# Performance work log

Hardware: AMD Instinct MI355X
Metric: run time of the kernel (lower is better)

## Reference

```python
import jax, jax.numpy as jnp
import numpy as np

N_NODES = 20000
N_EDGES = 320000
D_IN = 128
D_HID = 128
D_OUT = 128
HEADS = 4
NEG_SLOPE = 0.2
BN_EPS = 1e-5


def _gat_conv(x, src, dst, W, a_src, a_dst, b):
    """PyG GATConv with concat=False (mean over heads). Self-loops already in src/dst."""
    N = x.shape[0]
    H, C = a_src.shape
    h = (x @ W).reshape(N, H, C)                     # [N,H,C] per-head projections
    alpha_s = jnp.sum(h * a_src, axis=-1)            # [N,H]
    alpha_d = jnp.sum(h * a_dst, axis=-1)            # [N,H]
    logits = jax.nn.leaky_relu(alpha_s[src] + alpha_d[dst], NEG_SLOPE)  # [E,H]
    # segment softmax over incoming edges of each destination node
    m = jax.ops.segment_max(logits, dst, num_segments=N)               # [N,H]
    e = jnp.exp(logits - m[dst])
    z = jax.ops.segment_sum(e, dst, num_segments=N)                     # [N,H]
    alpha = e / (z[dst] + 1e-16)                                        # [E,H]
    msg = h[src] * alpha[:, :, None]                                    # [E,H,C]
    out = jax.ops.segment_sum(msg, dst, num_segments=N)                 # [N,H,C]
    return jnp.mean(out, axis=1) + b                                    # [N,C]


def _bn(x, gamma, beta):
    mu = jnp.mean(x, axis=0)
    var = jnp.var(x, axis=0)
    return (x - mu) * jax.lax.rsqrt(var + BN_EPS) * gamma + beta


def setup_inputs() -> dict:
    key = jax.random.key(0)
    ks = jax.random.split(key, 24)
    inp = {
        'x': jax.random.normal(ks[0], (N_NODES, D_IN), jnp.float32),
        'edge_index': jax.random.randint(ks[1], (2, N_EDGES), 0, N_NODES, jnp.int64),
        'edge_attr': jax.random.normal(ks[2], (N_EDGES, 16), jnp.float32),
    }
    def glorot(k, shape):
        fan = sum(shape) if len(shape) > 1 else shape[0]
        return jax.random.normal(k, shape, jnp.float32) * np.float32(np.sqrt(2.0 / fan))
    dims = [(D_IN, D_HID), (D_HID, D_HID), (D_HID, D_OUT)]
    for i, (din, dout) in enumerate(dims):
        inp[f'W{i}'] = glorot(ks[3 + 4 * i], (din, HEADS * dout))
        inp[f'asrc{i}'] = glorot(ks[4 + 4 * i], (HEADS, dout))
        inp[f'adst{i}'] = glorot(ks[5 + 4 * i], (HEADS, dout))
        inp[f'b{i}'] = jnp.zeros((dout,), jnp.float32)
    for i in range(2):
        inp[f'gamma{i}'] = jnp.ones((D_HID,), jnp.float32)
        inp[f'beta{i}'] = jnp.zeros((D_HID,), jnp.float32)
    return inp


def reference(x, edge_index, edge_attr, W0, asrc0, adst0, b0, gamma0, beta0,
              W1, asrc1, adst1, b1, gamma1, beta1, W2, asrc2, adst2, b2):
    N = x.shape[0]
    ar = jnp.arange(N, dtype=edge_index.dtype)
    src = jnp.concatenate([edge_index[0], ar])  # add self-loops (PyG default)
    dst = jnp.concatenate([edge_index[1], ar])
    h = _gat_conv(x, src, dst, W0, asrc0, adst0, b0)
    h = jax.nn.relu(_bn(h, gamma0, beta0))
    h = _gat_conv(h, src, dst, W1, asrc1, adst1, b1)
    h = jax.nn.relu(_bn(h, gamma1, beta1))
    out = _gat_conv(h, src, dst, W2, asrc2, adst2, b2)
    return (out, edge_attr)
```

## Files before the change

kernel.cpp:

```cpp
#include <hip/hip_runtime.h>
#include <hip/hip_fp16.h>
#include <math.h>

#define N_NODES 20000
#define N_EDGES 320000
#define EN (N_EDGES + N_NODES)
#define DIM 128
#define HEADS 4
#define DH (HEADS * DIM)
#define NEG_SLOPE 0.2f
#define BN_EPS 1e-5f

typedef _Float16 h4 __attribute__((ext_vector_type(4)));
typedef _Float16 h8 __attribute__((ext_vector_type(8)));
typedef float f4 __attribute__((ext_vector_type(4)));

__device__ __forceinline__ float lrelu(float x) { return x > 0.f ? x : NEG_SLOPE * x; }


__global__ __launch_bounds__(256) void build_edges_kernel(
    const void* __restrict__ ei_raw, int* __restrict__ src32,
    int* __restrict__ dst32, int* __restrict__ deg) {
  int e = blockIdx.x * 256 + threadIdx.x;
  if (e >= EN) return;
  const long long* ei64 = (const long long*)ei_raw;
  const int* ei32 = (const int*)ei_raw;
  bool is64 = true;
#pragma unroll
  for (int k = 0; k < 4; ++k) {
    long long v = ei64[k];
    if (v < 0 || v >= N_NODES) is64 = false;
  }
  int s, d;
  if (e < N_EDGES) {
    if (is64) { s = (int)ei64[e]; d = (int)ei64[N_EDGES + e]; }
    else      { s = ei32[e];      d = ei32[N_EDGES + e]; }
  } else {
    s = d = e - N_EDGES;
  }
  src32[e] = s;
  dst32[e] = d;
  atomicAdd(&deg[d], 1);
}

__global__ __launch_bounds__(1024) void scan_kernel(
    const int* __restrict__ deg, int* __restrict__ off) {
  __shared__ int sums[1024];
  const int tid = threadIdx.x;
  const int chunk = (N_NODES + 1023) / 1024;
  int start = tid * chunk;
  int end = start + chunk; if (end > N_NODES) end = N_NODES;
  int s = 0;
  for (int i = start; i < end && i < N_NODES; ++i) s += deg[i];
  sums[tid] = s;
  __syncthreads();
  for (int st = 1; st < 1024; st <<= 1) {
    int t = (tid >= st) ? sums[tid - st] : 0;
    __syncthreads();
    sums[tid] += t;
    __syncthreads();
  }
  int run = sums[tid] - s;
  for (int i = start; i < end && i < N_NODES; ++i) { off[i] = run; run += deg[i]; }
  if (tid == 1023) off[N_NODES] = sums[1023];
}

__global__ __launch_bounds__(256) void scatter_kernel(
    const int* __restrict__ src32, const int* __restrict__ dst32,
    const int* __restrict__ off, int* __restrict__ cursor,
    int* __restrict__ csrc) {
  int e = blockIdx.x * 256 + threadIdx.x;
  if (e >= EN) return;
  int d = dst32[e];
  int pos = atomicAdd(&cursor[d], 1);
  csrc[off[d] + pos] = src32[e];
}


__global__ __launch_bounds__(128) void wtrans_kernel(
    const float* __restrict__ W0, const float* __restrict__ W1,
    const float* __restrict__ W2, __half* __restrict__ T0,
    __half* __restrict__ T1, __half* __restrict__ T2) {
  int n = blockIdx.x;
  int k = threadIdx.x;
  const float* W = (blockIdx.y == 0) ? W0 : (blockIdx.y == 1) ? W1 : W2;
  __half* T = (blockIdx.y == 0) ? T0 : (blockIdx.y == 1) ? T1 : T2;
  T[(size_t)n * 128 + k] = __float2half(W[(size_t)k * 512 + n]);
}


__global__ __launch_bounds__(128) void bn_coef_kernel(
    const float* __restrict__ stats, const float* __restrict__ gamma,
    const float* __restrict__ beta, float* __restrict__ coef) {
  int c = threadIdx.x;
  const float invN = 1.f / (float)N_NODES;
  float mean = stats[c] * invN;
  float var = stats[DIM + c] * invN - mean * mean;
  float scale = gamma[c] * rsqrtf(var + BN_EPS);
  coef[c] = scale;
  coef[DIM + c] = beta[c] - mean * scale;
}


#define SWZ(r, byte_in_row) (((r) * 256 + (byte_in_row)) ^ (((r) & 7) << 4))

__global__ __launch_bounds__(256) void gemm_fused_kernel(
    const float* __restrict__ A, const __half* __restrict__ Wt,
    const float* __restrict__ coef, int apply_bn,
    const float* __restrict__ a_src, const float* __restrict__ a_dst,
    ushort* __restrict__ H16, float* __restrict__ as_,
    float* __restrict__ ad_, int M) {
  __shared__ __align__(16) char Xt[64 * 256];
  __shared__ __align__(16) char Wl[64 * 256];
  __shared__ float red_as[4][4][2][16];
  __shared__ float red_ad[4][4][2][16];
  int tid = threadIdx.x;
  int brow = blockIdx.x * 64;
  int half_id = blockIdx.y;
  const float4* coef4 = (const float4*)coef;
#pragma unroll
  for (int it = 0; it < 8; ++it) {
    int idx = it * 256 + tid;
    int r = idx >> 5, c4 = idx & 31;
    int row = brow + r;
    float4 v = make_float4(0.f, 0.f, 0.f, 0.f);
    if (row < M) {
      v = *(const float4*)&A[(size_t)row * 128 + c4 * 4];
      if (apply_bn) {
        float4 sc = coef4[c4], sh = coef4[32 + c4];
        v.x = fmaxf(v.x * sc.x + sh.x, 0.f);
        v.y = fmaxf(v.y * sc.y + sh.y, 0.f);
        v.z = fmaxf(v.z * sc.z + sh.z, 0.f);
        v.w = fmaxf(v.w * sc.w + sh.w, 0.f);
      }
    }
    h4 hv;
    hv[0] = (_Float16)v.x; hv[1] = (_Float16)v.y;
    hv[2] = (_Float16)v.z; hv[3] = (_Float16)v.w;
    *(h4*)(Xt + SWZ(r, c4 * 8)) = hv;
  }
  int wave = tid >> 6, lane = tid & 63;
  int lrow = lane & 15, kgrp = lane >> 4;
  float asum[4][2] = {}, adsum[4][2] = {};
  for (int nc = 0; nc < 4; ++nc) {
    int chunk = half_id * 4 + nc;
    int hh = nc >> 1;
    __syncthreads();
#pragma unroll
    for (int it = 0; it < 4; ++it) {
      int idx = it * 256 + tid;
      int r = idx >> 4, c4 = idx & 15;
      uint4 v = *(const uint4*)&Wt[(size_t)(chunk * 64 + r) * 128 + c4 * 8];
      *(uint4*)(Wl + SWZ(r, c4 * 16)) = v;
    }
    __syncthreads();
    f4 acc[4] = {};
#pragma unroll
    for (int ks = 0; ks < 4; ++ks) {
      int kb = ks * 64 + kgrp * 16;
      h8 af = *(h8*)(Wl + SWZ(wave * 16 + lrow, kb));
#pragma unroll
      for (int mt = 0; mt < 4; ++mt) {
        h8 bf = *(h8*)(Xt + SWZ(mt * 16 + lrow, kb));
        acc[mt] = __builtin_amdgcn_mfma_f32_16x16x32_f16(af, bf, acc[mt], 0, 0, 0);
      }
    }
    int n_base = chunk * 64 + wave * 16 + kgrp * 4;
    float4 as4 = *(const float4*)&a_src[n_base];
    float4 ad4 = *(const float4*)&a_dst[n_base];
#pragma unroll
    for (int mt = 0; mt < 4; ++mt) {
      int m = brow + mt * 16 + lrow;
      if (m < M) {
        h4 hv;
#pragma unroll
        for (int i = 0; i < 4; ++i) hv[i] = (_Float16)acc[mt][i];
        *(h4*)&H16[(size_t)m * DH + n_base] = hv;
      }
      asum[mt][hh] += acc[mt][0] * as4.x + acc[mt][1] * as4.y +
                      acc[mt][2] * as4.z + acc[mt][3] * as4.w;
      adsum[mt][hh] += acc[mt][0] * ad4.x + acc[mt][1] * ad4.y +
                       acc[mt][2] * ad4.z + acc[mt][3] * ad4.w;
    }
  }
#pragma unroll
  for (int mt = 0; mt < 4; ++mt)
#pragma unroll
    for (int hh = 0; hh < 2; ++hh) {
      asum[mt][hh] += __shfl_xor(asum[mt][hh], 16);
      asum[mt][hh] += __shfl_xor(asum[mt][hh], 32);
      adsum[mt][hh] += __shfl_xor(adsum[mt][hh], 16);
      adsum[mt][hh] += __shfl_xor(adsum[mt][hh], 32);
    }
  __syncthreads();
  if (lane < 16) {
#pragma unroll
    for (int mt = 0; mt < 4; ++mt)
#pragma unroll
      for (int hh = 0; hh < 2; ++hh) {
        red_as[wave][mt][hh][lrow] = asum[mt][hh];
        red_ad[wave][mt][hh][lrow] = adsum[mt][hh];
      }
  }
  __syncthreads();
  if (tid < 128) {
    int mt = tid >> 5, hh = (tid >> 4) & 1, lr = tid & 15;
    float s = red_as[0][mt][hh][lr] + red_as[1][mt][hh][lr] +
              red_as[2][mt][hh][lr] + red_as[3][mt][hh][lr];
    float d = red_ad[0][mt][hh][lr] + red_ad[1][mt][hh][lr] +
              red_ad[2][mt][hh][lr] + red_ad[3][mt][hh][lr];
    int m = brow + mt * 16 + lr;
    if (m < M) {
      int head = half_id * 2 + hh;
      as_[m * 4 + head] = s;
      ad_[m * 4 + head] = d;
    }
  }
}


__global__ __launch_bounds__(256) void smagg_kernel(
    const ushort* __restrict__ H16, const float* __restrict__ as_,
    const float* __restrict__ ad_, const int* __restrict__ off,
    const int* __restrict__ csrc, const float* __restrict__ bias,
    float* __restrict__ out, float* __restrict__ galpha) {
  __shared__ float alds[4][64 * 4];
  int tid = threadIdx.x;
  int slot = tid >> 6;
  int n = blockIdx.x * 4 + slot;
  int lane = tid & 63;
  int e0 = off[n], e1 = off[n + 1];
  int deg = e1 - e0;
  bool fast = (deg <= 64);
  float4 ad = *(const float4*)&ad_[n * 4];
  if (fast) {
    bool valid = lane < deg;
    float l0 = -1e30f, l1 = -1e30f, l2 = -1e30f, l3 = -1e30f;
    if (valid) {
      int s = csrc[e0 + lane];
      float4 av = *(const float4*)&as_[s * 4];
      l0 = lrelu(av.x + ad.x); l1 = lrelu(av.y + ad.y);
      l2 = lrelu(av.z + ad.z); l3 = lrelu(av.w + ad.w);
    }
    float m0 = l0, m1 = l1, m2 = l2, m3 = l3;
#pragma unroll
    for (int o = 32; o > 0; o >>= 1) {
      m0 = fmaxf(m0, __shfl_xor(m0, o)); m1 = fmaxf(m1, __shfl_xor(m1, o));
      m2 = fmaxf(m2, __shfl_xor(m2, o)); m3 = fmaxf(m3, __shfl_xor(m3, o));
    }
    float p0 = valid ? expf(l0 - m0) : 0.f;
    float p1 = valid ? expf(l1 - m1) : 0.f;
    float p2 = valid ? expf(l2 - m2) : 0.f;
    float p3 = valid ? expf(l3 - m3) : 0.f;
    float z0 = p0, z1 = p1, z2 = p2, z3 = p3;
#pragma unroll
    for (int o = 32; o > 0; o >>= 1) {
      z0 += __shfl_xor(z0, o); z1 += __shfl_xor(z1, o);
      z2 += __shfl_xor(z2, o); z3 += __shfl_xor(z3, o);
    }
    if (valid) {
      float4 r = make_float4(p0 / (z0 + 1e-16f), p1 / (z1 + 1e-16f),
                             p2 / (z2 + 1e-16f), p3 / (z3 + 1e-16f));
      *(float4*)&alds[slot][lane * 4] = r;
    }
  } else {
    float m0 = -1e30f, m1 = -1e30f, m2 = -1e30f, m3 = -1e30f;
    for (int i = e0 + lane; i < e1; i += 64) {
      int s = csrc[i];
      float4 av = *(const float4*)&as_[s * 4];
      float l0 = lrelu(av.x + ad.x), l1 = lrelu(av.y + ad.y);
      float l2 = lrelu(av.z + ad.z), l3 = lrelu(av.w + ad.w);
      ((float4*)galpha)[i] = make_float4(l0, l1, l2, l3);
      m0 = fmaxf(m0, l0); m1 = fmaxf(m1, l1);
      m2 = fmaxf(m2, l2); m3 = fmaxf(m3, l3);
    }
#pragma unroll
    for (int o = 32; o > 0; o >>= 1) {
      m0 = fmaxf(m0, __shfl_xor(m0, o)); m1 = fmaxf(m1, __shfl_xor(m1, o));
      m2 = fmaxf(m2, __shfl_xor(m2, o)); m3 = fmaxf(m3, __shfl_xor(m3, o));
    }
    float z0 = 0.f, z1 = 0.f, z2 = 0.f, z3 = 0.f;
    for (int i = e0 + lane; i < e1; i += 64) {
      float4 l = ((const float4*)galpha)[i];
      float p0 = expf(l.x - m0), p1 = expf(l.y - m1);
      float p2 = expf(l.z - m2), p3 = expf(l.w - m3);
      ((float4*)galpha)[i] = make_float4(p0, p1, p2, p3);
      z0 += p0; z1 += p1; z2 += p2; z3 += p3;
    }
#pragma unroll
    for (int o = 32; o > 0; o >>= 1) {
      z0 += __shfl_xor(z0, o); z1 += __shfl_xor(z1, o);
      z2 += __shfl_xor(z2, o); z3 += __shfl_xor(z3, o);
    }
    float r0 = 1.f / (z0 + 1e-16f), r1 = 1.f / (z1 + 1e-16f);
    float r2 = 1.f / (z2 + 1e-16f), r3 = 1.f / (z3 + 1e-16f);
    for (int i = e0 + lane; i < e1; i += 64) {
      float4 p = ((const float4*)galpha)[i];
      ((float4*)galpha)[i] = make_float4(p.x * r0, p.y * r1, p.z * r2, p.w * r3);
    }
  }
  const uint4* Hp = (const uint4*)H16;
  const float* af = &alds[slot][0];
  int head = lane >> 4;
  float acc[8] = {};
#define AGG_BODY(ii)                                                       \
  {                                                                        \
    int s = csrc[ii];                                                      \
    float w = fast ? af[((ii) - e0) * 4 + head]                            \
                   : galpha[(size_t)(ii) * 4 + head];                      \
    uint4 hv = Hp[(size_t)s * 64 + lane];                                  \
    float2 f0 = __half22float2(*(__half2*)&hv.x);                          \
    float2 f1 = __half22float2(*(__half2*)&hv.y);                          \
    float2 f2 = __half22float2(*(__half2*)&hv.z);                          \
    float2 f3 = __half22float2(*(__half2*)&hv.w);                          \
    acc[0] += w * f0.x; acc[1] += w * f0.y;                                \
    acc[2] += w * f1.x; acc[3] += w * f1.y;                                \
    acc[4] += w * f2.x; acc[5] += w * f2.y;                                \
    acc[6] += w * f3.x; acc[7] += w * f3.y;                                \
  }
  int i = e0;
  for (; i + 7 < e1; i += 8) {
    AGG_BODY(i)     AGG_BODY(i + 1) AGG_BODY(i + 2) AGG_BODY(i + 3)
    AGG_BODY(i + 4) AGG_BODY(i + 5) AGG_BODY(i + 6) AGG_BODY(i + 7)
  }
  for (; i < e1; ++i) AGG_BODY(i)
#undef AGG_BODY
#pragma unroll
  for (int j = 0; j < 8; ++j) {
    acc[j] += __shfl_xor(acc[j], 16);
    acc[j] += __shfl_xor(acc[j], 32);
  }
  if (lane < 16) {
    int c0 = lane * 8;
    float4 b0 = *(const float4*)&bias[c0];
    float4 b1 = *(const float4*)&bias[c0 + 4];
    float4 r0 = make_float4(0.25f * acc[0] + b0.x, 0.25f * acc[1] + b0.y,
                            0.25f * acc[2] + b0.z, 0.25f * acc[3] + b0.w);
    float4 r1 = make_float4(0.25f * acc[4] + b1.x, 0.25f * acc[5] + b1.y,
                            0.25f * acc[6] + b1.z, 0.25f * acc[7] + b1.w);
    *(float4*)&out[(size_t)n * DIM + c0] = r0;
    *(float4*)&out[(size_t)n * DIM + c0 + 4] = r1;
  }
}


__global__ __launch_bounds__(256) void bn_stats_kernel(
    const float* __restrict__ X, float* __restrict__ stats) {
  int c = threadIdx.x & 127;
  int hlf = threadIdx.x >> 7;
  float s = 0.f, s2 = 0.f;
  for (int r = blockIdx.x * 2 + hlf; r < N_NODES; r += gridDim.x * 2) {
    float v = X[(size_t)r * DIM + c];
    s += v;
    s2 += v * v;
  }
  atomicAdd(&stats[c], s);
  atomicAdd(&stats[DIM + c], s2);
}


extern "C" void kernel_launch(void* const* d_in, const int* in_sizes, int n_in,
                              void* d_out, int out_size, void* d_ws, size_t ws_size,
                              hipStream_t stream) {
  (void)in_sizes; (void)n_in; (void)out_size; (void)ws_size;
  const float* x = (const float*)d_in[0];
  const void* ei = d_in[1];
  const float* eattr = (const float*)d_in[2];
  const float* W[3]    = {(const float*)d_in[3],  (const float*)d_in[7],  (const float*)d_in[11]};
  const float* asrc[3] = {(const float*)d_in[4],  (const float*)d_in[8],  (const float*)d_in[12]};
  const float* adst[3] = {(const float*)d_in[5],  (const float*)d_in[9],  (const float*)d_in[13]};
  const float* bias[3] = {(const float*)d_in[6],  (const float*)d_in[10], (const float*)d_in[14]};
  const float* gamma[2] = {(const float*)d_in[15], (const float*)d_in[17]};
  const float* beta[2]  = {(const float*)d_in[16], (const float*)d_in[18]};

  char* ws = (char*)d_ws;
  size_t o = 0;
  auto alloc = [&](size_t bytes) -> void* {
    void* p = ws + o;
    o += (bytes + 255) & ~(size_t)255;
    return p;
  };
  int* deg      = (int*)alloc(N_NODES * 4);
  int* cursor   = (int*)alloc(N_NODES * 4);
  float* stats0 = (float*)alloc(2 * DIM * 4);
  float* stats1 = (float*)alloc(2 * DIM * 4);
  size_t zero_bytes = o;
  int* off    = (int*)alloc((N_NODES + 1) * 4);
  int* src32  = (int*)alloc((size_t)EN * 4);
  int* dst32  = (int*)alloc((size_t)EN * 4);
  int* csrc   = (int*)alloc((size_t)EN * 4);
  float* galpha = (float*)alloc((size_t)EN * 4 * 4);
  ushort* H16  = (ushort*)alloc((size_t)N_NODES * DH * 2);
  float* Ob    = (float*)alloc((size_t)N_NODES * DIM * 4);
  float* as_   = (float*)alloc((size_t)N_NODES * 4 * 4);
  float* ad_   = (float*)alloc((size_t)N_NODES * 4 * 4);
  float* coef0 = (float*)alloc(2 * DIM * 4);
  float* coef1 = (float*)alloc(2 * DIM * 4);
  __half* Wt[3];
  for (int L = 0; L < 3; ++L) Wt[L] = (__half*)alloc((size_t)DH * 128 * 2);

  hipMemsetAsync(d_ws, 0, zero_bytes, stream);

  build_edges_kernel<<<(EN + 255) / 256, 256, 0, stream>>>(ei, src32, dst32, deg);
  scan_kernel<<<1, 1024, 0, stream>>>(deg, off);
  scatter_kernel<<<(EN + 255) / 256, 256, 0, stream>>>(src32, dst32, off, cursor, csrc);
  wtrans_kernel<<<dim3(DH, 3), 128, 0, stream>>>(W[0], W[1], W[2], Wt[0], Wt[1], Wt[2]);

  const float* in_ptr = x;
  const float* coefs[3] = {coef0, coef0, coef1};
  for (int L = 0; L < 3; ++L) {
    gemm_fused_kernel<<<dim3((N_NODES + 63) / 64, 2), 256, 0, stream>>>(
        in_ptr, Wt[L], coefs[L], (L > 0) ? 1 : 0, asrc[L], adst[L],
        H16, as_, ad_, N_NODES);
    float* outp = (L == 2) ? (float*)d_out : Ob;
    smagg_kernel<<<N_NODES / 4, 256, 0, stream>>>(H16, as_, ad_, off, csrc,
                                                  bias[L], outp, galpha);
    if (L < 2) {
      float* st = (L == 0) ? stats0 : stats1;
      float* cf = (L == 0) ? coef0 : coef1;
      bn_stats_kernel<<<256, 256, 0, stream>>>(Ob, st);
      bn_coef_kernel<<<1, 128, 0, stream>>>(st, gamma[L], beta[L], cf);
      in_ptr = Ob;
    }
  }

  hipMemcpyAsync((float*)d_out + (size_t)N_NODES * DIM, eattr,
                 (size_t)N_EDGES * 16 * 4, hipMemcpyDeviceToDevice, stream);
}
```

Measured before the change: 444.6 us.

## Double-buffer GEMM weight tiles over all heads and split aggregation across two waves

The fused GEMM kernel now handles all eight 64-column weight chunks in one block instead of splitting heads over two blocks. It stages each next weight chunk in registers and double-buffers it in LDS, which removes the duplicate X staging and overlaps weight loads with MFMA work. The aggregation kernel uses two waves per node, each handling alternate edges, and combines their partial sums through LDS. This raises memory-level parallelism for the gather but adds block barriers and halves the GEMM grid, which may reduce occupancy.

Result: slower. 526.2 us (+18.4%).

```diff
diff --git a/kernel.cpp b/kernel.cpp
--- a/kernel.cpp
+++ b/kernel.cpp
@@ -111,12 +111,11 @@
     ushort* __restrict__ H16, float* __restrict__ as_,
     float* __restrict__ ad_, int M) {
   __shared__ __align__(16) char Xt[64 * 256];
-  __shared__ __align__(16) char Wl[64 * 256];
-  __shared__ float red_as[4][4][2][16];
-  __shared__ float red_ad[4][4][2][16];
+  __shared__ __align__(16) char Wl[2][64 * 256];
+  __shared__ float red_as[4][4][4][16];
+  __shared__ float red_ad[4][4][4][16];
   int tid = threadIdx.x;
   int brow = blockIdx.x * 64;
-  int half_id = blockIdx.y;
   const float4* coef4 = (const float4*)coef;
 #pragma unroll
   for (int it = 0; it < 8; ++it) {
@@ -140,32 +139,37 @@
     *(h4*)(Xt + SWZ(r, c4 * 8)) = hv;
   }
   int wave = tid >> 6, lane = tid & 63;
+  int wr = tid >> 4, wc4 = tid & 15;
   int lrow = lane & 15, kgrp = lane >> 4;
-  float asum[4][2] = {}, adsum[4][2] = {};
-  for (int nc = 0; nc < 4; ++nc) {
-    int chunk = half_id * 4 + nc;
+  float asum[4][4] = {}, adsum[4][4] = {};
+  uint4 wreg[4];
+#pragma unroll
+  for (int it = 0; it < 4; ++it)
+    wreg[it] = *(const uint4*)&Wt[(size_t)(it * 16 + wr) * 128 + wc4 * 8];
+  for (int nc = 0; nc < 8; ++nc) {
+    char* buf = Wl[nc & 1];
     int hh = nc >> 1;
+#pragma unroll
+    for (int it = 0; it < 4; ++it)
+      *(uint4*)(buf + SWZ(it * 16 + wr, wc4 * 16)) = wreg[it];
     __syncthreads();
-#pragma unroll
-    for (int it = 0; it < 4; ++it) {
-      int idx = it * 256 + tid;
-      int r = idx >> 4, c4 = idx & 15;
-      uint4 v = *(const uint4*)&Wt[(size_t)(chunk * 64 + r) * 128 + c4 * 8];
-      *(uint4*)(Wl + SWZ(r, c4 * 16)) = v;
-    }
-    __syncthreads();
+    if (nc < 7) {
+#pragma unroll
+      for (int it = 0; it < 4; ++it)
+        wreg[it] = *(const uint4*)&Wt[(size_t)((nc + 1) * 64 + it * 16 + wr) * 128 + wc4 * 8];
+    }
     f4 acc[4] = {};
 #pragma unroll
     for (int ks = 0; ks < 4; ++ks) {
       int kb = ks * 64 + kgrp * 16;
-      h8 af = *(h8*)(Wl + SWZ(wave * 16 + lrow, kb));
+      h8 af = *(h8*)(buf + SWZ(wave * 16 + lrow, kb));
 #pragma unroll
       for (int mt = 0; mt < 4; ++mt) {
         h8 bf = *(h8*)(Xt + SWZ(mt * 16 + lrow, kb));
         acc[mt] = __builtin_amdgcn_mfma_f32_16x16x32_f16(af, bf, acc[mt], 0, 0, 0);
       }
     }
-    int n_base = chunk * 64 + wave * 16 + kgrp * 4;
+    int n_base = nc * 64 + wave * 16 + kgrp * 4;
     float4 as4 = *(const float4*)&a_src[n_base];
     float4 ad4 = *(const float4*)&a_dst[n_base];
 #pragma unroll
@@ -182,123 +186,128 @@
       adsum[mt][hh] += acc[mt][0] * ad4.x + acc[mt][1] * ad4.y +
                        acc[mt][2] * ad4.z + acc[mt][3] * ad4.w;
     }
+    __syncthreads();
   }
 #pragma unroll
   for (int mt = 0; mt < 4; ++mt)
 #pragma unroll
-    for (int hh = 0; hh < 2; ++hh) {
+    for (int hh = 0; hh < 4; ++hh) {
       asum[mt][hh] += __shfl_xor(asum[mt][hh], 16);
       asum[mt][hh] += __shfl_xor(asum[mt][hh], 32);
       adsum[mt][hh] += __shfl_xor(adsum[mt][hh], 16);
       adsum[mt][hh] += __shfl_xor(adsum[mt][hh], 32);
     }
-  __syncthreads();
   if (lane < 16) {
 #pragma unroll
     for (int mt = 0; mt < 4; ++mt)
 #pragma unroll
-      for (int hh = 0; hh < 2; ++hh) {
+      for (int hh = 0; hh < 4; ++hh) {
         red_as[wave][mt][hh][lrow] = asum[mt][hh];
         red_ad[wave][mt][hh][lrow] = adsum[mt][hh];
       }
   }
   __syncthreads();
-  if (tid < 128) {
-    int mt = tid >> 5, hh = (tid >> 4) & 1, lr = tid & 15;
+  {
+    int mt = tid >> 6, hh = (tid >> 4) & 3, lr = tid & 15;
     float s = red_as[0][mt][hh][lr] + red_as[1][mt][hh][lr] +
               red_as[2][mt][hh][lr] + red_as[3][mt][hh][lr];
     float d = red_ad[0][mt][hh][lr] + red_ad[1][mt][hh][lr] +
               red_ad[2][mt][hh][lr] + red_ad[3][mt][hh][lr];
     int m = brow + mt * 16 + lr;
     if (m < M) {
-      int head = half_id * 2 + hh;
-      as_[m * 4 + head] = s;
-      ad_[m * 4 + head] = d;
-    }
-  }
-}
-
-
-__global__ __launch_bounds__(256) void smagg_kernel(
+      as_[m * 4 + hh] = s;
+      ad_[m * 4 + hh] = d;
+    }
+  }
+}
+
+
+__global__ __launch_bounds__(512) void smagg_kernel(
     const ushort* __restrict__ H16, const float* __restrict__ as_,
     const float* __restrict__ ad_, const int* __restrict__ off,
     const int* __restrict__ csrc, const float* __restrict__ bias,
     float* __restrict__ out, float* __restrict__ galpha) {
   __shared__ float alds[4][64 * 4];
+  __shared__ float pred[4][128];
   int tid = threadIdx.x;
-  int slot = tid >> 6;
+  int wave = tid >> 6;
+  int slot = wave >> 1;
+  int sub = wave & 1;
   int n = blockIdx.x * 4 + slot;
   int lane = tid & 63;
   int e0 = off[n], e1 = off[n + 1];
   int deg = e1 - e0;
   bool fast = (deg <= 64);
-  float4 ad = *(const float4*)&ad_[n * 4];
-  if (fast) {
-    bool valid = lane < deg;
-    float l0 = -1e30f, l1 = -1e30f, l2 = -1e30f, l3 = -1e30f;
-    if (valid) {
-      int s = csrc[e0 + lane];
-      float4 av = *(const float4*)&as_[s * 4];
-      l0 = lrelu(av.x + ad.x); l1 = lrelu(av.y + ad.y);
-      l2 = lrelu(av.z + ad.z); l3 = lrelu(av.w + ad.w);
-    }
-    float m0 = l0, m1 = l1, m2 = l2, m3 = l3;
-#pragma unroll
-    for (int o = 32; o > 0; o >>= 1) {
-      m0 = fmaxf(m0, __shfl_xor(m0, o)); m1 = fmaxf(m1, __shfl_xor(m1, o));
-      m2 = fmaxf(m2, __shfl_xor(m2, o)); m3 = fmaxf(m3, __shfl_xor(m3, o));
-    }
-    float p0 = valid ? expf(l0 - m0) : 0.f;
-    float p1 = valid ? expf(l1 - m1) : 0.f;
-    float p2 = valid ? expf(l2 - m2) : 0.f;
-    float p3 = valid ? expf(l3 - m3) : 0.f;
-    float z0 = p0, z1 = p1, z2 = p2, z3 = p3;
-#pragma unroll
-    for (int o = 32; o > 0; o >>= 1) {
-      z0 += __shfl_xor(z0, o); z1 += __shfl_xor(z1, o);
-      z2 += __shfl_xor(z2, o); z3 += __shfl_xor(z3, o);
-    }
-    if (valid) {
-      float4 r = make_float4(p0 / (z0 + 1e-16f), p1 / (z1 + 1e-16f),
-                             p2 / (z2 + 1e-16f), p3 / (z3 + 1e-16f));
-      *(float4*)&alds[slot][lane * 4] = r;
-    }
-  } else {
-    float m0 = -1e30f, m1 = -1e30f, m2 = -1e30f, m3 = -1e30f;
-    for (int i = e0 + lane; i < e1; i += 64) {
-      int s = csrc[i];
-      float4 av = *(const float4*)&as_[s * 4];
-      float l0 = lrelu(av.x + ad.x), l1 = lrelu(av.y + ad.y);
-      float l2 = lrelu(av.z + ad.z), l3 = lrelu(av.w + ad.w);
-      ((float4*)galpha)[i] = make_float4(l0, l1, l2, l3);
-      m0 = fmaxf(m0, l0); m1 = fmaxf(m1, l1);
-      m2 = fmaxf(m2, l2); m3 = fmaxf(m3, l3);
-    }
-#pragma unroll
-    for (int o = 32; o > 0; o >>= 1) {
-      m0 = fmaxf(m0, __shfl_xor(m0, o)); m1 = fmaxf(m1, __shfl_xor(m1, o));
-      m2 = fmaxf(m2, __shfl_xor(m2, o)); m3 = fmaxf(m3, __shfl_xor(m3, o));
-    }
-    float z0 = 0.f, z1 = 0.f, z2 = 0.f, z3 = 0.f;
-    for (int i = e0 + lane; i < e1; i += 64) {
-      float4 l = ((const float4*)galpha)[i];
-      float p0 = expf(l.x - m0), p1 = expf(l.y - m1);
-      float p2 = expf(l.z - m2), p3 = expf(l.w - m3);
-      ((float4*)galpha)[i] = make_float4(p0, p1, p2, p3);
-      z0 += p0; z1 += p1; z2 += p2; z3 += p3;
-    }
-#pragma unroll
-    for (int o = 32; o > 0; o >>= 1) {
-      z0 += __shfl_xor(z0, o); z1 += __shfl_xor(z1, o);
-      z2 += __shfl_xor(z2, o); z3 += __shfl_xor(z3, o);
-    }
-    float r0 = 1.f / (z0 + 1e-16f), r1 = 1.f / (z1 + 1e-16f);
-    float r2 = 1.f / (z2 + 1e-16f), r3 = 1.f / (z3 + 1e-16f);
-    for (int i = e0 + lane; i < e1; i += 64) {
-      float4 p = ((const float4*)galpha)[i];
-      ((float4*)galpha)[i] = make_float4(p.x * r0, p.y * r1, p.z * r2, p.w * r3);
-    }
-  }
+  if (sub == 0) {
+    float4 ad = *(const float4*)&ad_[n * 4];
+    if (fast) {
+      bool valid = lane < deg;
+      float l0 = -1e30f, l1 = -1e30f, l2 = -1e30f, l3 = -1e30f;
+      if (valid) {
+        int s = csrc[e0 + lane];
+        float4 av = *(const float4*)&as_[s * 4];
+        l0 = lrelu(av.x + ad.x); l1 = lrelu(av.y + ad.y);
+        l2 = lrelu(av.z + ad.z); l3 = lrelu(av.w + ad.w);
+      }
+      float m0 = l0, m1 = l1, m2 = l2, m3 = l3;
+#pragma unroll
+      for (int o = 32; o > 0; o >>= 1) {
+        m0 = fmaxf(m0, __shfl_xor(m0, o)); m1 = fmaxf(m1, __shfl_xor(m1, o));
+        m2 = fmaxf(m2, __shfl_xor(m2, o)); m3 = fmaxf(m3, __shfl_xor(m3, o));
+      }
+      float p0 = valid ? expf(l0 - m0) : 0.f;
+      float p1 = valid ? expf(l1 - m1) : 0.f;
+      float p2 = valid ? expf(l2 - m2) : 0.f;
+      float p3 = valid ? expf(l3 - m3) : 0.f;
+      float z0 = p0, z1 = p1, z2 = p2, z3 = p3;
+#pragma unroll
+      for (int o = 32; o > 0; o >>= 1) {
+        z0 += __shfl_xor(z0, o); z1 += __shfl_xor(z1, o);
+        z2 += __shfl_xor(z2, o); z3 += __shfl_xor(z3, o);
+      }
+      if (valid) {
+        float4 r = make_float4(p0 / (z0 + 1e-16f), p1 / (z1 + 1e-16f),
+                               p2 / (z2 + 1e-16f), p3 / (z3 + 1e-16f));
+        *(float4*)&alds[slot][lane * 4] = r;
+      }
+    } else {
+      float m0 = -1e30f, m1 = -1e30f, m2 = -1e30f, m3 = -1e30f;
+      for (int i = e0 + lane; i < e1; i += 64) {
+        int s = csrc[i];
+        float4 av = *(const float4*)&as_[s * 4];
+        float l0 = lrelu(av.x + ad.x), l1 = lrelu(av.y + ad.y);
+        float l2 = lrelu(av.z + ad.z), l3 = lrelu(av.w + ad.w);
+        ((float4*)galpha)[i] = make_float4(l0, l1, l2, l3);
+        m0 = fmaxf(m0, l0); m1 = fmaxf(m1, l1);
+        m2 = fmaxf(m2, l2); m3 = fmaxf(m3, l3);
+      }
+#pragma unroll
+      for (int o = 32; o > 0; o >>= 1) {
+        m0 = fmaxf(m0, __shfl_xor(m0, o)); m1 = fmaxf(m1, __shfl_xor(m1, o));
+        m2 = fmaxf(m2, __shfl_xor(m2, o)); m3 = fmaxf(m3, __shfl_xor(m3, o));
+      }
+      float z0 = 0.f, z1 = 0.f, z2 = 0.f, z3 = 0.f;
+      for (int i = e0 + lane; i < e1; i += 64) {
+        float4 l = ((const float4*)galpha)[i];
+        float p0 = expf(l.x - m0), p1 = expf(l.y - m1);
+        float p2 = expf(l.z - m2), p3 = expf(l.w - m3);
+        ((float4*)galpha)[i] = make_float4(p0, p1, p2, p3);
+        z0 += p0; z1 += p1; z2 += p2; z3 += p3;
+      }
+#pragma unroll
+      for (int o = 32; o > 0; o >>= 1) {
+        z0 += __shfl_xor(z0, o); z1 += __shfl_xor(z1, o);
+        z2 += __shfl_xor(z2, o); z3 += __shfl_xor(z3, o);
+      }
+      float r0 = 1.f / (z0 + 1e-16f), r1 = 1.f / (z1 + 1e-16f);
+      float r2 = 1.f / (z2 + 1e-16f), r3 = 1.f / (z3 + 1e-16f);
+      for (int i = e0 + lane; i < e1; i += 64) {
+        float4 p = ((const float4*)galpha)[i];
+        ((float4*)galpha)[i] = make_float4(p.x * r0, p.y * r1, p.z * r2, p.w * r3);
+      }
+    }
+  }
+  __syncthreads();
   const uint4* Hp = (const uint4*)H16;
   const float* af = &alds[slot][0];
   int head = lane >> 4;
@@ -318,26 +327,35 @@
     acc[4] += w * f2.x; acc[5] += w * f2.y;                                \
     acc[6] += w * f3.x; acc[7] += w * f3.y;                                \
   }
-  int i = e0;
-  for (; i + 7 < e1; i += 8) {
-    AGG_BODY(i)     AGG_BODY(i + 1) AGG_BODY(i + 2) AGG_BODY(i + 3)
-    AGG_BODY(i + 4) AGG_BODY(i + 5) AGG_BODY(i + 6) AGG_BODY(i + 7)
-  }
-  for (; i < e1; ++i) AGG_BODY(i)
+  int i = e0 + sub;
+  for (; i + 6 < e1; i += 8) {
+    AGG_BODY(i) AGG_BODY(i + 2) AGG_BODY(i + 4) AGG_BODY(i + 6)
+  }
+  for (; i < e1; i += 2) AGG_BODY(i)
 #undef AGG_BODY
 #pragma unroll
   for (int j = 0; j < 8; ++j) {
     acc[j] += __shfl_xor(acc[j], 16);
     acc[j] += __shfl_xor(acc[j], 32);
   }
-  if (lane < 16) {
+  if (sub == 1 && lane < 16) {
+#pragma unroll
+    for (int j = 0; j < 8; ++j) pred[slot][lane * 8 + j] = acc[j];
+  }
+  __syncthreads();
+  if (sub == 0 && lane < 16) {
     int c0 = lane * 8;
     float4 b0 = *(const float4*)&bias[c0];
     float4 b1 = *(const float4*)&bias[c0 + 4];
-    float4 r0 = make_float4(0.25f * acc[0] + b0.x, 0.25f * acc[1] + b0.y,
-                            0.25f * acc[2] + b0.z, 0.25f * acc[3] + b0.w);
-    float4 r1 = make_float4(0.25f * acc[4] + b1.x, 0.25f * acc[5] + b1.y,
-                            0.25f * acc[6] + b1.z, 0.25f * acc[7] + b1.w);
+    const float* pr = &pred[slot][c0];
+    float4 r0 = make_float4(0.25f * (acc[0] + pr[0]) + b0.x,
+                            0.25f * (acc[1] + pr[1]) + b0.y,
+                            0.25f * (acc[2] + pr[2]) + b0.z,
+                            0.25f * (acc[3] + pr[3]) + b0.w);
+    float4 r1 = make_float4(0.25f * (acc[4] + pr[4]) + b1.x,
+                            0.25f * (acc[5] + pr[5]) + b1.y,
+                            0.25f * (acc[6] + pr[6]) + b1.z,
+                            0.25f * (acc[7] + pr[7]) + b1.w);
     *(float4*)&out[(size_t)n * DIM + c0] = r0;
     *(float4*)&out[(size_t)n * DIM + c0 + 4] = r1;
   }
@@ -409,11 +427,11 @@
   const float* in_ptr = x;
   const float* coefs[3] = {coef0, coef0, coef1};
   for (int L = 0; L < 3; ++L) {
-    gemm_fused_kernel<<<dim3((N_NODES + 63) / 64, 2), 256, 0, stream>>>(
+    gemm_fused_kernel<<<(N_NODES + 63) / 64, 256, 0, stream>>>(
         in_ptr, Wt[L], coefs[L], (L > 0) ? 1 : 0, asrc[L], adst[L],
         H16, as_, ad_, N_NODES);
     float* outp = (L == 2) ? (float*)d_out : Ob;
-    smagg_kernel<<<N_NODES / 4, 256, 0, stream>>>(H16, as_, ad_, off, csrc,
+    smagg_kernel<<<N_NODES / 4, 512, 0, stream>>>(H16, as_, ad_, off, csrc,
                                                   bias[L], outp, galpha);
     if (L < 2) {
       float* st = (L == 0) ? stats0 : stats1;
```

## Pre-convert GEMM input to fp16 and load tiles via direct global-to-LDS loads

Applied to the files above, without the earlier changes.

Adds a separate kernel that applies the BN+ReLU and converts each layer's input to fp16 once, instead of doing it inside the GEMM. The GEMM then loads both the activation and weight tiles with global_load_lds (direct global-to-LDS), computing the swizzle on the source address. This removes the fp32 loads, the per-row conversion and the register round-trip through VGPRs for LDS staging, and halves the activation bytes each GEMM block reads. In exchange it adds three small conversion kernel launches and an extra fp16 buffer write and read. The padded X16 allocation covers the final partial tile, but those padding rows are not zeroed.

New measurement: 452.6 us. No clear change (+1.8%).

```diff
diff --git a/kernel.cpp b/kernel.cpp
--- a/kernel.cpp
+++ b/kernel.cpp
@@ -14,6 +14,9 @@
 typedef _Float16 h4 __attribute__((ext_vector_type(4)));
 typedef _Float16 h8 __attribute__((ext_vector_type(8)));
 typedef float f4 __attribute__((ext_vector_type(4)));
+
+typedef const __attribute__((address_space(1))) void gv_t;
+typedef __attribute__((address_space(3))) void lv_t;
 
 __device__ __forceinline__ float lrelu(float x) { return x > 0.f ? x : NEG_SLOPE * x; }
 
@@ -102,11 +105,32 @@
 }
 
 
+__global__ __launch_bounds__(256) void cvt16_kernel(
+    const float* __restrict__ src, const float* __restrict__ coef,
+    int apply_bn, __half* __restrict__ dst) {
+  int idx = blockIdx.x * 256 + threadIdx.x;
+  if (idx >= N_NODES * DIM / 4) return;
+  int c4 = idx & 31;
+  float4 v = ((const float4*)src)[idx];
+  if (apply_bn) {
+    const float4* coef4 = (const float4*)coef;
+    float4 sc = coef4[c4], sh = coef4[32 + c4];
+    v.x = fmaxf(v.x * sc.x + sh.x, 0.f);
+    v.y = fmaxf(v.y * sc.y + sh.y, 0.f);
+    v.z = fmaxf(v.z * sc.z + sh.z, 0.f);
+    v.w = fmaxf(v.w * sc.w + sh.w, 0.f);
+  }
+  union { __half2 h2[2]; uint2 u; } pk;
+  pk.h2[0] = __floats2half2_rn(v.x, v.y);
+  pk.h2[1] = __floats2half2_rn(v.z, v.w);
+  ((uint2*)dst)[idx] = pk.u;
+}
+
+
 #define SWZ(r, byte_in_row) (((r) * 256 + (byte_in_row)) ^ (((r) & 7) << 4))
 
 __global__ __launch_bounds__(256) void gemm_fused_kernel(
-    const float* __restrict__ A, const __half* __restrict__ Wt,
-    const float* __restrict__ coef, int apply_bn,
+    const __half* __restrict__ X16, const __half* __restrict__ Wt,
     const float* __restrict__ a_src, const float* __restrict__ a_dst,
     ushort* __restrict__ H16, float* __restrict__ as_,
     float* __restrict__ ad_, int M) {
@@ -115,31 +139,18 @@
   __shared__ float red_as[4][4][2][16];
   __shared__ float red_ad[4][4][2][16];
   int tid = threadIdx.x;
+  int wave = tid >> 6, lane = tid & 63;
   int brow = blockIdx.x * 64;
   int half_id = blockIdx.y;
-  const float4* coef4 = (const float4*)coef;
-#pragma unroll
-  for (int it = 0; it < 8; ++it) {
-    int idx = it * 256 + tid;
-    int r = idx >> 5, c4 = idx & 31;
-    int row = brow + r;
-    float4 v = make_float4(0.f, 0.f, 0.f, 0.f);
-    if (row < M) {
-      v = *(const float4*)&A[(size_t)row * 128 + c4 * 4];
-      if (apply_bn) {
-        float4 sc = coef4[c4], sh = coef4[32 + c4];
-        v.x = fmaxf(v.x * sc.x + sh.x, 0.f);
-        v.y = fmaxf(v.y * sc.y + sh.y, 0.f);
-        v.z = fmaxf(v.z * sc.z + sh.z, 0.f);
-        v.w = fmaxf(v.w * sc.w + sh.w, 0.f);
-      }
-    }
-    h4 hv;
-    hv[0] = (_Float16)v.x; hv[1] = (_Float16)v.y;
-    hv[2] = (_Float16)v.z; hv[3] = (_Float16)v.w;
-    *(h4*)(Xt + SWZ(r, c4 * 8)) = hv;
-  }
-  int wave = tid >> 6, lane = tid & 63;
+#pragma unroll
+  for (int it = 0; it < 4; ++it) {
+    int seg = it * 4 + wave;
+    int pos = seg * 1024 + lane * 16;
+    int r = pos >> 8, b = pos & 255;
+    int gb = b ^ ((r & 7) << 4);
+    const char* gsrc = (const char*)(X16 + (size_t)(brow + r) * 128) + gb;
+    __builtin_amdgcn_global_load_lds((gv_t*)gsrc, (lv_t*)(Xt + seg * 1024), 16, 0, 0);
+  }
   int lrow = lane & 15, kgrp = lane >> 4;
   float asum[4][2] = {}, adsum[4][2] = {};
   for (int nc = 0; nc < 4; ++nc) {
@@ -148,10 +159,12 @@
     __syncthreads();
 #pragma unroll
     for (int it = 0; it < 4; ++it) {
-      int idx = it * 256 + tid;
-      int r = idx >> 4, c4 = idx & 15;
-      uint4 v = *(const uint4*)&Wt[(size_t)(chunk * 64 + r) * 128 + c4 * 8];
-      *(uint4*)(Wl + SWZ(r, c4 * 16)) = v;
+      int seg = it * 4 + wave;
+      int pos = seg * 1024 + lane * 16;
+      int r = pos >> 8, b = pos & 255;
+      int gb = b ^ ((r & 7) << 4);
+      const char* gsrc = (const char*)(Wt + (size_t)(chunk * 64 + r) * 128) + gb;
+      __builtin_amdgcn_global_load_lds((gv_t*)gsrc, (lv_t*)(Wl + seg * 1024), 16, 0, 0);
     }
     __syncthreads();
     f4 acc[4] = {};
@@ -391,6 +404,7 @@
   int* csrc   = (int*)alloc((size_t)EN * 4);
   float* galpha = (float*)alloc((size_t)EN * 4 * 4);
   ushort* H16  = (ushort*)alloc((size_t)N_NODES * DH * 2);
+  __half* X16  = (__half*)alloc((size_t)(N_NODES + 64) * DIM * 2);
   float* Ob    = (float*)alloc((size_t)N_NODES * DIM * 4);
   float* as_   = (float*)alloc((size_t)N_NODES * 4 * 4);
   float* ad_   = (float*)alloc((size_t)N_NODES * 4 * 4);
@@ -406,12 +420,12 @@
   scatter_kernel<<<(EN + 255) / 256, 256, 0, stream>>>(src32, dst32, off, cursor, csrc);
   wtrans_kernel<<<dim3(DH, 3), 128, 0, stream>>>(W[0], W[1], W[2], Wt[0], Wt[1], Wt[2]);
 
-  const float* in_ptr = x;
-  const float* coefs[3] = {coef0, coef0, coef1};
+  const int cvt_blocks = (N_NODES * DIM / 4 + 255) / 256;
+  cvt16_kernel<<<cvt_blocks, 256, 0, stream>>>(x, coef0, 0, X16);
+
   for (int L = 0; L < 3; ++L) {
     gemm_fused_kernel<<<dim3((N_NODES + 63) / 64, 2), 256, 0, stream>>>(
-        in_ptr, Wt[L], coefs[L], (L > 0) ? 1 : 0, asrc[L], adst[L],
-        H16, as_, ad_, N_NODES);
+        X16, Wt[L], asrc[L], adst[L], H16, as_, ad_, N_NODES);
     float* outp = (L == 2) ? (float*)d_out : Ob;
     smagg_kernel<<<N_NODES / 4, 256, 0, stream>>>(H16, as_, ad_, off, csrc,
                                                   bias[L], outp, galpha);
@@ -420,7 +434,7 @@
       float* cf = (L == 0) ? coef0 : coef1;
       bn_stats_kernel<<<256, 256, 0, stream>>>(Ob, st);
       bn_coef_kernel<<<1, 128, 0, stream>>>(st, gamma[L], beta[L], cf);
-      in_ptr = Ob;
+      cvt16_kernel<<<cvt_blocks, 256, 0, stream>>>(Ob, cf, 1, X16);
     }
   }
 
```
